# Performance work log

Measured on AMD Instinct MI355X. Metric: run time of the kernel, lower is better.

The kernel has to match this reference:

```python
import jax, jax.numpy as jnp
import numpy as np

N, E, IN_DIM, HID = 8192, 65536, 128, 64
BN_EPS = 1e-5


def setup_inputs() -> dict:
    key = jax.random.key(0)
    ks = jax.random.split(key, 16)
    inp = {
        'h': jax.random.normal(ks[0], (N, IN_DIM), dtype=jnp.float32),
        'src': jax.random.randint(ks[1], (E,), 0, N, dtype=jnp.int32),
        'dst': jax.random.randint(ks[2], (E,), 0, N, dtype=jnp.int32),
        'proj1_w': jax.random.normal(ks[3], (HID * HID, IN_DIM), dtype=jnp.float32) * 0.02,
        'proj1_b': jax.random.normal(ks[4], (HID * HID,), dtype=jnp.float32) * 0.02,
        'proj2_w': jax.random.normal(ks[5], (HID, IN_DIM), dtype=jnp.float32) * 0.02,
        'proj2_b': jax.random.normal(ks[6], (HID,), dtype=jnp.float32) * 0.02,
        'conv_w': jax.random.normal(ks[7], (1, 2, 3), dtype=jnp.float32) * 0.2,
        'conv_b': jax.random.normal(ks[8], (1,), dtype=jnp.float32) * 0.2,
        'ep2_w': jax.random.normal(ks[9], (HID, IN_DIM), dtype=jnp.float32) * 0.02,
        'ep2_b': jax.random.normal(ks[10], (HID,), dtype=jnp.float32) * 0.02,
        'ep3_w': jax.random.normal(ks[11], (HID, HID), dtype=jnp.float32) * 0.02,
        'ep3_b': jax.random.normal(ks[12], (HID,), dtype=jnp.float32) * 0.02,
        'bn_gamma': jnp.ones((HID,), dtype=jnp.float32),
        'bn_beta': jnp.zeros((HID,), dtype=jnp.float32),
        'bn_mean': jnp.zeros((HID,), dtype=jnp.float32),
        'bn_var': jnp.ones((HID,), dtype=jnp.float32),
    }
    return inp


def reference(h, src, dst, proj1_w, proj1_b, proj2_w, proj2_b, conv_w, conv_b,
              ep2_w, ep2_b, ep3_w, ep3_b, bn_gamma, bn_beta, bn_mean, bn_var):
    # ---- local edge path: cat(src,dst) -> Conv1d(2->1,k3,p1) -> Linear ----
    edge = jnp.stack([h[src], h[dst]], axis=1)  # [E, 2, in_dim]
    conv = jax.lax.conv_general_dilated(
        edge, conv_w, window_strides=(1,), padding=[(1, 1)],
        dimension_numbers=('NCW', 'OIW', 'NCW'))  # [E, 1, in_dim]
    conv = conv + conv_b[None, :, None]
    lr_e_local = jnp.squeeze(conv, axis=1) @ ep2_w.T + ep2_b  # [E, hid]

    # ---- global edge path (SDDMM form of the dense NxN*hid mm) ----
    # torch: mm.view(N,hid,N).permute(0,2,1)[src,dst] == A[src] @ p2[dst]
    A = (h @ proj1_w.T + proj1_b).reshape(-1, HID, HID)  # [N, hid, hid]
    p2 = h @ proj2_w.T + proj2_b                          # [N, hid]
    lr_e_global = jnp.einsum('ejd,ed->ej', A[src], p2[dst])  # [E, hid]
    lr_e_global = lr_e_global @ ep3_w.T + ep3_b

    e = lr_e_local + lr_e_global
    # BatchNorm1d in eval mode (running stats), then ReLU; dropout is a no-op in eval.
    e = (e - bn_mean) * jax.lax.rsqrt(bn_var + BN_EPS) * bn_gamma + bn_beta
    return jax.nn.relu(e)
```

## Files before the change

### kernel.cpp

```cpp
#include <hip/hip_runtime.h>
#include <stdint.h>

#define NN   8192
#define EE   65536
#define IND  128
#define HID  64
#define NB   4096
#define BCAP 64

typedef __attribute__((ext_vector_type(8))) short short8;
typedef __attribute__((ext_vector_type(4))) float f32x4;
typedef _Float16 h8f __attribute__((ext_vector_type(8)));

__device__ __forceinline__ unsigned short f2bf(float f) {
  unsigned int x = __float_as_uint(f);
  x += 0x7fffu + ((x >> 16) & 1u);
  return (unsigned short)(x >> 16);
}
__device__ __forceinline__ unsigned short f2h(float v) {
  return __builtin_bit_cast(unsigned short, (_Float16)v);
}

#define GLOAD_LDS16(g, l) __builtin_amdgcn_global_load_lds( \
    (const __attribute__((address_space(1))) unsigned int*)(g), \
    (__attribute__((address_space(3))) unsigned int*)(l), 16, 0, 0)

__global__ __launch_bounds__(256) void k_prep(const float* __restrict__ h,
                                              const float* __restrict__ proj1_w,
                                              const float* __restrict__ proj1_b,
                                              const float* __restrict__ ep3_w,
                                              const float* __restrict__ proj2_w,
                                              const float* __restrict__ ep2_w,
                                              const float* __restrict__ ep2_b,
                                              const float* __restrict__ conv_w,
                                              const float* __restrict__ conv_b,
                                              const float* __restrict__ ep3_b,
                                              const float* __restrict__ bn_g,
                                              const float* __restrict__ bn_b,
                                              const float* __restrict__ bn_m,
                                              const float* __restrict__ bn_v,
                                              unsigned short* __restrict__ h_bf,
                                              int* __restrict__ cnt,
                                              unsigned short* __restrict__ Wp_bf,
                                              float* __restrict__ bp,
                                              unsigned short* __restrict__ Wn,
                                              float* __restrict__ consts) {
  __shared__ union {
    struct { float ep3t[64][65]; float Ps[64][128]; float p1bs[64]; } w;
    float red[256];
  } sm;
  const int b = blockIdx.x;
  const int t = threadIdx.x;
  if (b < 512) {
    if (b < 8) *(int4*)(cnt + (size_t)b * 1024 + t * 4) = make_int4(0, 0, 0, 0);
    const int idx = b * 256 + t;
    const float4* s = (const float4*)h + (size_t)idx * 2;
    float4 a = s[0], bb = s[1];
    uint4 p;
    p.x = (unsigned)f2bf(a.x) | ((unsigned)f2bf(a.y) << 16);
    p.y = (unsigned)f2bf(a.z) | ((unsigned)f2bf(a.w) << 16);
    p.z = (unsigned)f2bf(bb.x) | ((unsigned)f2bf(bb.y) << 16);
    p.w = (unsigned)f2bf(bb.z) | ((unsigned)f2bf(bb.w) << 16);
    *(uint4*)(h_bf + (size_t)idx * 8) = p;
  } else if (b < 576) {
    const int d = b - 512;
#pragma unroll
    for (int s = 0; s < 16; ++s) {
      int idx = s * 256 + t;
      sm.w.ep3t[idx & 63][idx >> 6] = ep3_w[idx];
    }
#pragma unroll
    for (int s = 0; s < 8; ++s) {
      int idx = s * 256 + t;
      int j = idx >> 5, kq = idx & 31;
      *(float4*)&sm.w.Ps[j][kq * 4] = *(const float4*)(proj1_w + (size_t)(j * 64 + d) * IND + kq * 4);
    }
    if (t < 64) sm.w.p1bs[t] = proj1_b[t * 64 + d];
    __syncthreads();
    const int i = t & 63, kq = t >> 6;
    float acc[32];
#pragma unroll
    for (int kk = 0; kk < 32; ++kk) acc[kk] = 0.f;
    for (int j = 0; j < 64; ++j) {
      float e = sm.w.ep3t[j][i];
#pragma unroll
      for (int k4 = 0; k4 < 8; ++k4) {
        float4 pv = *(const float4*)&sm.w.Ps[j][kq * 32 + k4 * 4];
        acc[k4 * 4 + 0] += e * pv.x; acc[k4 * 4 + 1] += e * pv.y;
        acc[k4 * 4 + 2] += e * pv.z; acc[k4 * 4 + 3] += e * pv.w;
      }
    }
    unsigned short* dstp = Wp_bf + (size_t)(i * 64 + d) * IND + kq * 32;
#pragma unroll
    for (int kk = 0; kk < 32; kk += 2) {
      unsigned int p = (unsigned)f2bf(acc[kk]) | ((unsigned)f2bf(acc[kk + 1]) << 16);
      *(unsigned int*)(dstp + kk) = p;
    }
    if (kq == 0) {
      float bsum = 0.f;
      for (int j = 0; j < 64; ++j) bsum += sm.w.ep3t[j][i] * sm.w.p1bs[j];
      bp[i * 64 + d] = bsum;
    }
  } else {
    const int i = b - 576;
    const int x = t & 127;
    float u = 0.f, v = 0.f;
    for (int k = 0; k < 3; ++k) {
      int w = x + 1 - k;
      if (w >= 0 && w < IND) {
        float e = ep2_w[i * IND + w];
        u += conv_w[k] * e;
        v += conv_w[3 + k] * e;
      }
    }
    Wn[(size_t)i * IND + x]         = f2bf(proj2_w[i * IND + x]);
    Wn[(size_t)(64 + i) * IND + x]  = f2bf(u);
    Wn[(size_t)(128 + i) * IND + x] = f2bf(v);
    sm.red[t] = ep2_w[i * IND + x];
    __syncthreads();
    for (int s = 128; s > 0; s >>= 1) {
      if (t < s) sm.red[t] += sm.red[t + s];
      __syncthreads();
    }
    if (t == 0) {
      float scale = bn_g[i] * rsqrtf(bn_v[i] + 1e-5f);
      float shift = bn_b[i] - bn_m[i] * scale;
      float cb = conv_b[0] * sm.red[0] * 0.5f + ep2_b[i] + ep3_b[i];
      consts[i] = scale;
      consts[64 + i] = shift;
      consts[128 + i] = cb;
    }
  }
}

__global__ __launch_bounds__(256) void k_mm(const unsigned short* __restrict__ hbf,
                                            const unsigned short* __restrict__ Wbf,
                                            const float* __restrict__ bp,
                                            const unsigned short* __restrict__ Wn,
                                            const float* __restrict__ proj2_b,
                                            const int* __restrict__ src,
                                            const int* __restrict__ dst,
                                            int* __restrict__ cnt,
                                            int2* __restrict__ bucket,
                                            unsigned short* __restrict__ Bm,
                                            unsigned short* __restrict__ pld,
                                            float* __restrict__ Ls32) {
  __shared__ unsigned char sm[49152];
  const int t = threadIdx.x;
  if (blockIdx.x < 4096) {
    unsigned char* smA = sm;
    unsigned char* smB = sm + 32768;
    const int n0 = (blockIdx.x & 63) * 64, m0 = (blockIdx.x >> 6) * 128;
    const unsigned short* gA = hbf + (size_t)m0 * IND;
    const unsigned short* gB = Wbf + (size_t)n0 * IND;
#pragma unroll
    for (int s = 0; s < 8; ++s) {
      int p = s * 256 + t;
      int gp = (p & ~15) | ((p ^ (p >> 4)) & 15);
      GLOAD_LDS16(gA + gp * 8, smA + p * 16);
    }
#pragma unroll
    for (int s = 0; s < 4; ++s) {
      int p = s * 256 + t;
      int gp = (p & ~15) | ((p ^ (p >> 4)) & 15);
      GLOAD_LDS16(gB + gp * 8, smB + p * 16);
    }
    __syncthreads();
    const int w = t >> 6, lane = t & 63;
    const int wr = w >> 1, wc = w & 1;
    const int lrow = lane & 15, quad = lane >> 4;
    f32x4 acc[4][2] = {};
#pragma unroll
    for (int ks = 0; ks < 4; ++ks) {
      short8 af[4], bfr[2];
#pragma unroll
      for (int a = 0; a < 4; ++a) {
        int row = wr * 64 + a * 16 + lrow;
        int chunk = (ks * 4 + quad) ^ (row & 15);
        af[a] = *(const short8*)(smA + row * 256 + chunk * 16);
      }
#pragma unroll
      for (int b = 0; b < 2; ++b) {
        int row = wc * 32 + b * 16 + lrow;
        int chunk = (ks * 4 + quad) ^ (row & 15);
        bfr[b] = *(const short8*)(smB + row * 256 + chunk * 16);
      }
#pragma unroll
      for (int a = 0; a < 4; ++a)
#pragma unroll
        for (int b = 0; b < 2; ++b)
          acc[a][b] = __builtin_amdgcn_mfma_f32_16x16x32_bf16(af[a], bfr[b], acc[a][b], 0, 0, 0);
    }
    float bv[2];
#pragma unroll
    for (int b = 0; b < 2; ++b) bv[b] = bp[n0 + wc * 32 + b * 16 + lrow];
    __syncthreads();
#pragma unroll
    for (int a = 0; a < 4; ++a) {
      int R0 = wr * 64 + a * 16 + quad * 4;
#pragma unroll
      for (int b = 0; b < 2; ++b) {
        int C = wc * 32 + b * 16 + lrow;
#pragma unroll
        for (int v = 0; v < 4; ++v)
          *(unsigned short*)(sm + (size_t)(R0 + v) * 144 + C * 2) = f2h(acc[a][b][v] + bv[b]);
      }
    }
    __syncthreads();
#pragma unroll
    for (int s = 0; s < 4; ++s) {
      int p = s * 256 + t;
      int row = p >> 3, q = p & 7;
      uint4 val = *(const uint4*)(sm + (size_t)row * 144 + q * 16);
      *(uint4*)(Bm + (size_t)(m0 + row) * NB + n0 + q * 8) = val;
    }
  } else if (blockIdx.x < 4224) {
    unsigned char* smA = sm;
    unsigned char* smW = sm + 16384;
    const int m0 = (blockIdx.x - 4096) * 64;
#pragma unroll
    for (int s = 0; s < 4; ++s) {
      int p = s * 256 + t;
      int row = p >> 4, c = p & 15;
      int cs = c ^ (row & 15);
      GLOAD_LDS16(hbf + (size_t)(m0 + row) * IND + cs * 8, smA + p * 16);
    }
#pragma unroll
    for (int s = 0; s < 6; ++s) {
      int p = s * 256 + t;
      int row = p >> 4, c = p & 15;
      int cs = c ^ (row & 15);
      GLOAD_LDS16(Wn + (size_t)row * IND + cs * 8, smW + p * 16);
    }
    __syncthreads();
    const int w = t >> 6, lane = t & 63;
    const int lrow = lane & 15, quad = lane >> 4;
    const int row0 = m0 + w * 16 + quad * 4;
    for (int pass = 0; pass < 2; ++pass) {
      f32x4 acc[6] = {};
#pragma unroll
      for (int ks = 0; ks < 4; ++ks) {
        const int chunk = (ks * 4 + quad) ^ lrow;
        short8 af = *(const short8*)(smA + (w * 16 + lrow) * 256 + chunk * 16);
#pragma unroll
        for (int nl = 0; nl < 6; ++nl) {
          int rl = nl * 16 + lrow;
          int ch = (ks * 4 + quad) ^ (rl & 15);
          short8 bfr = *(const short8*)(smW + rl * 256 + ch * 16);
          acc[nl] = __builtin_amdgcn_mfma_f32_16x16x32_bf16(af, bfr, acc[nl], 0, 0, 0);
        }
      }
#pragma unroll
      for (int nl = 0; nl < 6; ++nl) {
        int n = pass * 6 + nl;
        int col = n * 16 + lrow;
        if (n < 4) {
          float b = proj2_b[col];
#pragma unroll
          for (int v = 0; v < 4; ++v)
            pld[(size_t)(row0 + v) * 128 + col] = f2h(acc[nl][v] + b);
        } else if (n < 8) {
          int c2 = col - 64;
#pragma unroll
          for (int v = 0; v < 4; ++v)
            Ls32[(size_t)(row0 + v) * HID + c2] = acc[nl][v];
        } else {
          int c2 = col - 128;
#pragma unroll
          for (int v = 0; v < 4; ++v)
            pld[(size_t)(row0 + v) * 128 + 64 + c2] = f2h(acc[nl][v]);
        }
      }
      if (pass == 0) {
        __syncthreads();
#pragma unroll
        for (int s = 0; s < 6; ++s) {
          int p = s * 256 + t;
          int row = p >> 4, c = p & 15;
          int cs = c ^ (row & 15);
          GLOAD_LDS16(Wn + (size_t)(96 + row) * IND + cs * 8, smW + p * 16);
        }
        __syncthreads();
      }
    }
  } else {
    const int e = (blockIdx.x - 4224) * 256 + t;
    const int s = src[e], d = dst[e];
    const int p = atomicAdd(&cnt[s], 1);
    if (p < BCAP) bucket[(size_t)s * BCAP + p] = make_int2(e, d);
  }
}

__global__ __launch_bounds__(256) void k_edge(const int* __restrict__ cnt,
                                              const int2* __restrict__ bucket,
                                              const unsigned short* __restrict__ Bm,
                                              const unsigned short* __restrict__ pld,
                                              const float* __restrict__ Ls32,
                                              const float* __restrict__ consts,
                                              float* __restrict__ out) {
  const int t = threadIdx.x;
  const int w = t >> 6, lane = t & 63;
  const int s = blockIdx.x * 4 + w;
  const int n = min(cnt[s], BCAP);
  if (n == 0) return;
  const int lrow = lane & 15, quad = lane >> 4;
  const unsigned short* Brow = Bm + (size_t)s * NB;
  h8f afr[4][2];
#pragma unroll
  for (int tt = 0; tt < 4; ++tt)
#pragma unroll
    for (int ks = 0; ks < 2; ++ks)
      afr[tt][ks] = *(const h8f*)(Brow + (tt * 16 + lrow) * 64 + ks * 32 + quad * 8);
  h8f idf[4];
#pragma unroll
  for (int tt = 0; tt < 4; ++tt) {
    int j = tt * 16 + lrow - (tt >> 1) * 32 - quad * 8;
    uint4 iw = make_uint4(0, 0, 0, 0);
    if (j >= 0 && j < 8) {
      unsigned val = 0x3C00u << ((j & 1) * 16);
      int jw = j >> 1;
      if (jw == 0) iw.x = val; else if (jw == 1) iw.y = val;
      else if (jw == 2) iw.z = val; else iw.w = val;
    }
    idf[tt] = __builtin_bit_cast(h8f, iw);
  }
  float4 sc4[4], sh4[4], cbl[4];
#pragma unroll
  for (int tt = 0; tt < 4; ++tt) {
    int ib = tt * 16 + quad * 4;
    sc4[tt] = *(const float4*)(consts + ib);
    sh4[tt] = *(const float4*)(consts + 64 + ib);
    float4 cb = *(const float4*)(consts + 128 + ib);
    float4 ls = *(const float4*)(Ls32 + (size_t)s * HID + ib);
    cbl[tt] = make_float4(cb.x + ls.x, cb.y + ls.y, cb.z + ls.z, cb.w + ls.w);
  }
  for (int b0 = 0; b0 < n; b0 += 16) {
    const int idx = b0 + lrow;
    const int2 ed = bucket[(size_t)s * BCAP + min(idx, n - 1)];
    const unsigned short* prow = pld + (size_t)ed.y * 128;
    h8f bf0 = *(const h8f*)(prow + quad * 8);
    h8f bf1 = *(const h8f*)(prow + 32 + quad * 8);
    h8f bl0 = *(const h8f*)(prow + 64 + quad * 8);
    h8f bl1 = *(const h8f*)(prow + 96 + quad * 8);
    f32x4 acc[4] = {};
#pragma unroll
    for (int tt = 0; tt < 4; ++tt) {
      acc[tt] = __builtin_amdgcn_mfma_f32_16x16x32_f16(afr[tt][0], bf0, acc[tt], 0, 0, 0);
      acc[tt] = __builtin_amdgcn_mfma_f32_16x16x32_f16(afr[tt][1], bf1, acc[tt], 0, 0, 0);
      acc[tt] = __builtin_amdgcn_mfma_f32_16x16x32_f16(idf[tt], (tt < 2) ? bl0 : bl1, acc[tt], 0, 0, 0);
    }
    if (idx < n) {
      float* orow = out + (size_t)ed.x * HID;
#pragma unroll
      for (int tt = 0; tt < 4; ++tt) {
        float4 o;
        o.x = fmaxf((acc[tt][0] + cbl[tt].x) * sc4[tt].x + sh4[tt].x, 0.f);
        o.y = fmaxf((acc[tt][1] + cbl[tt].y) * sc4[tt].y + sh4[tt].y, 0.f);
        o.z = fmaxf((acc[tt][2] + cbl[tt].z) * sc4[tt].z + sh4[tt].z, 0.f);
        o.w = fmaxf((acc[tt][3] + cbl[tt].w) * sc4[tt].w + sh4[tt].w, 0.f);
        *(float4*)(orow + tt * 16 + quad * 4) = o;
      }
    }
  }
}

extern "C" void kernel_launch(void* const* d_in, const int* in_sizes, int n_in,
                              void* d_out, int out_size, void* d_ws, size_t ws_size,
                              hipStream_t stream) {
  const float* h       = (const float*)d_in[0];
  const int*   src     = (const int*)d_in[1];
  const int*   dst     = (const int*)d_in[2];
  const float* proj1_w = (const float*)d_in[3];
  const float* proj1_b = (const float*)d_in[4];
  const float* proj2_w = (const float*)d_in[5];
  const float* proj2_b = (const float*)d_in[6];
  const float* conv_w  = (const float*)d_in[7];
  const float* conv_b  = (const float*)d_in[8];
  const float* ep2_w   = (const float*)d_in[9];
  const float* ep2_b   = (const float*)d_in[10];
  const float* ep3_w   = (const float*)d_in[11];
  const float* ep3_b   = (const float*)d_in[12];
  const float* bn_g    = (const float*)d_in[13];
  const float* bn_b    = (const float*)d_in[14];
  const float* bn_m    = (const float*)d_in[15];
  const float* bn_v    = (const float*)d_in[16];

  char* ws = (char*)d_ws;
  unsigned short* Wp_bf = (unsigned short*)ws;  ws += (size_t)NB * IND * 2;
  unsigned short* h_bf  = (unsigned short*)ws;  ws += (size_t)NN * IND * 2;
  float* bp     = (float*)ws;                   ws += (size_t)NB * 4;
  unsigned short* Wn = (unsigned short*)ws;     ws += (size_t)192 * IND * 2;
  float* consts = (float*)ws;                   ws += 1024;
  int* cnt      = (int*)ws;                     ws += 8192 * 4;
  int2* bucket  = (int2*)ws;                    ws += (size_t)NN * BCAP * 8;
  unsigned short* pld = (unsigned short*)ws;    ws += (size_t)NN * 128 * 2;
  float* Ls32   = (float*)ws;                   ws += (size_t)NN * HID * 4;
  unsigned short* Bm = (unsigned short*)ws;

  k_prep<<<640, 256, 0, stream>>>(h, proj1_w, proj1_b, ep3_w, proj2_w,
                                  ep2_w, ep2_b, conv_w, conv_b, ep3_b,
                                  bn_g, bn_b, bn_m, bn_v,
                                  h_bf, cnt, Wp_bf, bp, Wn, consts);
  k_mm<<<4480, 256, 0, stream>>>(h_bf, Wp_bf, bp, Wn, proj2_b, src, dst,
                                 cnt, bucket, Bm, pld, Ls32);
  k_edge<<<NN / 4, 256, 0, stream>>>(cnt, bucket, Bm, pld, Ls32, consts, (float*)d_out);
}
```

Before: 158.7 us.

## Split big projection GEMM into per-wave direct-load kernel, separate mid kernel

The large h·proj1 GEMM moves into its own kernel, k_bm. In it each wave computes an independent 32x64 tile, loading its operands straight from global memory into registers instead of staging a block-wide tile in LDS. LDS is used only for a small per-wave swizzled epilogue buffer that coalesces the fp16 stores. The small projection and edge-bucketing work moves to a separate k_mid launch. The aim is to cut LDS footprint and block-wide sync so occupancy rises, at the cost of more redundant global/L2 reads per wave and an extra kernel launch.

```diff
diff --git a/kernel.cpp b/kernel.cpp
--- a/kernel.cpp
+++ b/kernel.cpp
@@ -133,91 +133,73 @@
   }
 }
 
-__global__ __launch_bounds__(256) void k_mm(const unsigned short* __restrict__ hbf,
+__global__ __launch_bounds__(256) void k_bm(const unsigned short* __restrict__ hbf,
                                             const unsigned short* __restrict__ Wbf,
                                             const float* __restrict__ bp,
-                                            const unsigned short* __restrict__ Wn,
-                                            const float* __restrict__ proj2_b,
-                                            const int* __restrict__ src,
-                                            const int* __restrict__ dst,
-                                            int* __restrict__ cnt,
-                                            int2* __restrict__ bucket,
-                                            unsigned short* __restrict__ Bm,
-                                            unsigned short* __restrict__ pld,
-                                            float* __restrict__ Ls32) {
-  __shared__ unsigned char sm[49152];
+                                            unsigned short* __restrict__ Bm) {
+  __shared__ unsigned char ep[4][4096];
   const int t = threadIdx.x;
-  if (blockIdx.x < 4096) {
-    unsigned char* smA = sm;
-    unsigned char* smB = sm + 32768;
-    const int n0 = (blockIdx.x & 63) * 64, m0 = (blockIdx.x >> 6) * 128;
-    const unsigned short* gA = hbf + (size_t)m0 * IND;
-    const unsigned short* gB = Wbf + (size_t)n0 * IND;
-#pragma unroll
-    for (int s = 0; s < 8; ++s) {
-      int p = s * 256 + t;
-      int gp = (p & ~15) | ((p ^ (p >> 4)) & 15);
-      GLOAD_LDS16(gA + gp * 8, smA + p * 16);
-    }
-#pragma unroll
-    for (int s = 0; s < 4; ++s) {
-      int p = s * 256 + t;
-      int gp = (p & ~15) | ((p ^ (p >> 4)) & 15);
-      GLOAD_LDS16(gB + gp * 8, smB + p * 16);
-    }
-    __syncthreads();
-    const int w = t >> 6, lane = t & 63;
-    const int wr = w >> 1, wc = w & 1;
-    const int lrow = lane & 15, quad = lane >> 4;
-    f32x4 acc[4][2] = {};
-#pragma unroll
-    for (int ks = 0; ks < 4; ++ks) {
-      short8 af[4], bfr[2];
-#pragma unroll
-      for (int a = 0; a < 4; ++a) {
-        int row = wr * 64 + a * 16 + lrow;
-        int chunk = (ks * 4 + quad) ^ (row & 15);
-        af[a] = *(const short8*)(smA + row * 256 + chunk * 16);
-      }
-#pragma unroll
-      for (int b = 0; b < 2; ++b) {
-        int row = wc * 32 + b * 16 + lrow;
-        int chunk = (ks * 4 + quad) ^ (row & 15);
-        bfr[b] = *(const short8*)(smB + row * 256 + chunk * 16);
-      }
-#pragma unroll
-      for (int a = 0; a < 4; ++a)
-#pragma unroll
-        for (int b = 0; b < 2; ++b)
-          acc[a][b] = __builtin_amdgcn_mfma_f32_16x16x32_bf16(af[a], bfr[b], acc[a][b], 0, 0, 0);
-    }
-    float bv[2];
-#pragma unroll
-    for (int b = 0; b < 2; ++b) bv[b] = bp[n0 + wc * 32 + b * 16 + lrow];
-    __syncthreads();
-#pragma unroll
-    for (int a = 0; a < 4; ++a) {
-      int R0 = wr * 64 + a * 16 + quad * 4;
-#pragma unroll
-      for (int b = 0; b < 2; ++b) {
-        int C = wc * 32 + b * 16 + lrow;
-#pragma unroll
-        for (int v = 0; v < 4; ++v)
-          *(unsigned short*)(sm + (size_t)(R0 + v) * 144 + C * 2) = f2h(acc[a][b][v] + bv[b]);
-      }
-    }
-    __syncthreads();
-#pragma unroll
-    for (int s = 0; s < 4; ++s) {
-      int p = s * 256 + t;
-      int row = p >> 3, q = p & 7;
-      uint4 val = *(const uint4*)(sm + (size_t)row * 144 + q * 16);
-      *(uint4*)(Bm + (size_t)(m0 + row) * NB + n0 + q * 8) = val;
-    }
-  } else if (blockIdx.x < 4224) {
+  const int w = t >> 6, lane = t & 63;
+  const int lrow = lane & 15, quad = lane >> 4;
+  const int id = blockIdx.x * 4 + w;
+  const int m0 = (id >> 6) * 32;
+  const int n0 = (id & 63) * 64;
+  f32x4 acc[2][4] = {};
+#pragma unroll
+  for (int ks = 0; ks < 4; ++ks) {
+    short8 af[2], bf[4];
+#pragma unroll
+    for (int a = 0; a < 2; ++a)
+      af[a] = *(const short8*)(hbf + (size_t)(m0 + a * 16 + lrow) * IND + ks * 32 + quad * 8);
+#pragma unroll
+    for (int b = 0; b < 4; ++b)
+      bf[b] = *(const short8*)(Wbf + (size_t)(n0 + b * 16 + lrow) * IND + ks * 32 + quad * 8);
+#pragma unroll
+    for (int a = 0; a < 2; ++a)
+#pragma unroll
+      for (int b = 0; b < 4; ++b)
+        acc[a][b] = __builtin_amdgcn_mfma_f32_16x16x32_bf16(af[a], bf[b], acc[a][b], 0, 0, 0);
+  }
+  float bv[4];
+#pragma unroll
+  for (int b = 0; b < 4; ++b) bv[b] = bp[n0 + b * 16 + lrow];
+#pragma unroll
+  for (int a = 0; a < 2; ++a)
+#pragma unroll
+    for (int b = 0; b < 4; ++b)
+#pragma unroll
+      for (int v = 0; v < 4; ++v) {
+        int r = a * 16 + quad * 4 + v;
+        int c = b * 16 + lrow;
+        int kc = (c >> 3) ^ (r & 7);
+        *(unsigned short*)(ep[w] + r * 128 + kc * 16 + (c & 7) * 2) = f2h(acc[a][b][v] + bv[b]);
+      }
+  __syncthreads();
+#pragma unroll
+  for (int j = 0; j < 4; ++j) {
+    int r = lane >> 1;
+    int k = (lane & 1) * 4 + j;
+    int kc = k ^ (r & 7);
+    uint4 val = *(const uint4*)(ep[w] + r * 128 + kc * 16);
+    *(uint4*)(Bm + (size_t)(m0 + r) * NB + n0 + k * 8) = val;
+  }
+}
+
+__global__ __launch_bounds__(256) void k_mid(const unsigned short* __restrict__ hbf,
+                                             const unsigned short* __restrict__ Wn,
+                                             const float* __restrict__ proj2_b,
+                                             const int* __restrict__ src,
+                                             const int* __restrict__ dst,
+                                             int* __restrict__ cnt,
+                                             int2* __restrict__ bucket,
+                                             unsigned short* __restrict__ pld,
+                                             float* __restrict__ Ls32) {
+  __shared__ unsigned char sm[40960];
+  const int t = threadIdx.x;
+  if (blockIdx.x < 128) {
     unsigned char* smA = sm;
     unsigned char* smW = sm + 16384;
-    const int m0 = (blockIdx.x - 4096) * 64;
+    const int m0 = blockIdx.x * 64;
 #pragma unroll
     for (int s = 0; s < 4; ++s) {
       int p = s * 256 + t;
@@ -284,7 +266,7 @@
       }
     }
   } else {
-    const int e = (blockIdx.x - 4224) * 256 + t;
+    const int e = (blockIdx.x - 128) * 256 + t;
     const int s = src[e], d = dst[e];
     const int p = atomicAdd(&cnt[s], 1);
     if (p < BCAP) bucket[(size_t)s * BCAP + p] = make_int2(e, d);
@@ -401,7 +383,7 @@
                                   ep2_w, ep2_b, conv_w, conv_b, ep3_b,
                                   bn_g, bn_b, bn_m, bn_v,
                                   h_bf, cnt, Wp_bf, bp, Wn, consts);
-  k_mm<<<4480, 256, 0, stream>>>(h_bf, Wp_bf, bp, Wn, proj2_b, src, dst,
-                                 cnt, bucket, Bm, pld, Ls32);
+  k_bm<<<4096, 256, 0, stream>>>(h_bf, Wp_bf, bp, Bm);
+  k_mid<<<384, 256, 0, stream>>>(h_bf, Wn, proj2_b, src, dst, cnt, bucket, pld, Ls32);
   k_edge<<<NN / 4, 256, 0, stream>>>(cnt, bucket, Bm, pld, Ls32, consts, (float*)d_out);
 }
```

Result: slower. 199.9 us (+25.9%).
